# Performance work log

Measured on AMD Instinct MI355X. Metric: run time of the kernel, lower is better.

## Reference

```python
import jax, jax.numpy as jnp
import numpy as np
from jax.ops import segment_sum

N = 100000
E = 1600000
IN_C = 128
WIDTHS = [128, 64, 32, 16, 8]  # hidden_feats=128 -> /1,/2,/4,/8,/16


def setup_inputs() -> dict:
    key = jax.random.key(0)
    ks = jax.random.split(key, 12)
    x = jax.random.normal(ks[0], (N, IN_C), dtype=jnp.float32)
    edge_index = jax.random.randint(ks[1], (2, E), 0, N, dtype=jnp.int64)
    inp = {"x": x, "edge_index": edge_index}
    fan_in = [IN_C] + WIDTHS[:-1]
    for i, (fi, fo) in enumerate(zip(fan_in, WIDTHS)):
        # Glorot init like PyG GCNConv
        lim = float(np.sqrt(6.0 / (fi + fo)))
        inp[f"W{i+1}"] = jax.random.uniform(ks[2 + i], (fi, fo), dtype=jnp.float32, minval=-lim, maxval=lim)
        inp[f"b{i+1}"] = jnp.zeros((fo,), dtype=jnp.float32)
    return inp


def _gcn_norm(edge_index):
    # add self loops, compute D^{-1/2} (A+I) D^{-1/2} edge weights
    loops = jnp.arange(N, dtype=edge_index.dtype)
    src = jnp.concatenate([edge_index[0], loops])  # [E+N]
    dst = jnp.concatenate([edge_index[1], loops])
    deg = segment_sum(jnp.ones_like(dst, dtype=jnp.float32), dst, num_segments=N)
    dinv = jnp.where(deg > 0, jax.lax.rsqrt(jnp.maximum(deg, 1.0)), 0.0)
    norm = dinv[src] * dinv[dst]  # [E+N]
    return src, dst, norm


def _gcn_layer(x, W, b, src, dst, norm):
    h = x @ W                         # [N, Fout] linear transform first (PyG order)
    msg = h[src] * norm[:, None]      # gather + edge scaling, [E+N, Fout]
    out = segment_sum(msg, dst, num_segments=N)  # scatter-add aggregation
    return out + b


def reference(x, edge_index, W1, b1, W2, b2, W3, b3, W4, b4, W5, b5):
    src, dst, norm = _gcn_norm(edge_index)
    params = [(W1, b1), (W2, b2), (W3, b3), (W4, b4), (W5, b5)]
    h = x
    for W, b in params:
        h = jax.nn.relu(_gcn_layer(h, W, b, src, dst, norm))
    return h
```

## Files before the change

kernel.cpp:

```cpp
#include <hip/hip_runtime.h>
#include <hip/hip_bf16.h>
#include <hip/hip_fp16.h>


#define LDSE8  4096
#define LDSE16 2048
#define PCHUNK 4096
#define BNODES 512
#define MAXBUK 256

typedef float floatx4 __attribute__((ext_vector_type(4)));
typedef _Float16 f16x4 __attribute__((ext_vector_type(4)));
typedef _Float16 f16x8 __attribute__((ext_vector_type(8)));

__global__ __launch_bounds__(256) void k_bucket(const int* __restrict__ src,
                                                const int* __restrict__ dst,
                                                int2* __restrict__ pairs,
                                                int* __restrict__ bcnt,
                                                int E, int nbk, int CAP) {
    __shared__ int  hist[MAXBUK], pre[MAXBUK], cur[MAXBUK], gbase[MAXBUK], tmp[MAXBUK];
    __shared__ int2 arena[PCHUNK];
    const int tid = threadIdx.x;
    const int e0  = blockIdx.x * PCHUNK;
    const int m   = (E - e0 < PCHUNK) ? (E - e0) : PCHUNK;

    hist[tid] = 0;
    __syncthreads();

    int dl[PCHUNK / 256], sl[PCHUNK / 256], rl[PCHUNK / 256];
#pragma unroll
    for (int j = 0; j < PCHUNK / 256; ++j) {
        int i = j * 256 + tid;
        rl[j] = -1;
        if (i < m) {
            dl[j] = __builtin_nontemporal_load(&dst[e0 + i]);
            sl[j] = __builtin_nontemporal_load(&src[e0 + i]);
            rl[j] = dl[j] >> 9;
            atomicAdd(&hist[rl[j]], 1);
        }
    }
    __syncthreads();
    int v = hist[tid];
    tmp[tid] = v;
    __syncthreads();
    for (int off = 1; off < MAXBUK; off <<= 1) {
        int t = (tid >= off) ? tmp[tid - off] : 0;
        __syncthreads();
        tmp[tid] += t;
        __syncthreads();
    }
    pre[tid] = tmp[tid] - v;
    cur[tid] = 0;
    __syncthreads();
#pragma unroll
    for (int j = 0; j < PCHUNK / 256; ++j) {
        if (rl[j] >= 0) {
            int slot = pre[rl[j]] + atomicAdd(&cur[rl[j]], 1);
            arena[slot] = make_int2(dl[j], sl[j]);
        }
    }
    __syncthreads();
    if (tid < nbk && hist[tid] > 0) gbase[tid] = atomicAdd(&bcnt[tid], hist[tid]);
    __syncthreads();
    const int wave = tid >> 6, lane = tid & 63;
    for (int r = wave; r < nbk; r += 4) {
        int cnt = hist[r];
        if (cnt == 0) continue;
        int b0 = pre[r], g = gbase[r];
        for (int j = lane; j < cnt; j += 64)
            pairs[(size_t)r * CAP + g + j] = arena[b0 + j];
    }
}

__global__ void k_bscan(const int* __restrict__ bcnt, int* __restrict__ bbase,
                        int* __restrict__ offsets, int nbk, int n, int E) {
    __shared__ int tmp[MAXBUK];
    const int tid = threadIdx.x;
    int v = (tid < nbk) ? bcnt[tid] : 0;
    tmp[tid] = v;
    __syncthreads();
    for (int off = 1; off < MAXBUK; off <<= 1) {
        int t = (tid >= off) ? tmp[tid - off] : 0;
        __syncthreads();
        tmp[tid] += t;
        __syncthreads();
    }
    if (tid < nbk) bbase[tid] = tmp[tid] - v;
    if (tid == 0) offsets[n] = E;
}

__global__ __launch_bounds__(256) void k_sortfill(const int2* __restrict__ pairs,
                                                  const int* __restrict__ bcnt,
                                                  const int* __restrict__ bbase,
                                                  int* __restrict__ csr_src,
                                                  int* __restrict__ offsets,
                                                  float* __restrict__ dinv,
                                                  int n, int CAP) {
    __shared__ int hist[BNODES], lofs[BNODES], cur[BNODES], tmp[256];
    const int r    = blockIdx.x;
    const int tid  = threadIdx.x;
    const int m    = bcnt[r];
    const int base = bbase[r];
    const int node0 = r * BNODES;
    const int2* p = pairs + (size_t)r * CAP;

    for (int l = tid; l < BNODES; l += 256) hist[l] = 0;
    __syncthreads();
    for (int i = tid; i < m; i += 256)
        atomicAdd(&hist[p[i].x - node0], 1);
    __syncthreads();
    int a = hist[2 * tid], b = hist[2 * tid + 1];
    int s = a + b;
    tmp[tid] = s;
    __syncthreads();
    for (int off = 1; off < 256; off <<= 1) {
        int t = (tid >= off) ? tmp[tid - off] : 0;
        __syncthreads();
        tmp[tid] += t;
        __syncthreads();
    }
    int exc = tmp[tid] - s;
    lofs[2 * tid]     = exc;
    lofs[2 * tid + 1] = exc + a;
    cur[2 * tid] = 0;
    cur[2 * tid + 1] = 0;
    __syncthreads();
    for (int i = tid; i < m; i += 256) {
        int2 e = p[i];
        int l = e.x - node0;
        int pos = lofs[l] + atomicAdd(&cur[l], 1);
        csr_src[base + pos] = e.y;
    }
    for (int l = tid; l < BNODES; l += 256) {
        int node = node0 + l;
        if (node < n) {
            offsets[node] = base + lofs[l];
            dinv[node]    = rsqrtf((float)(hist[l] + 1));
        }
    }
}

template <int FIN, int FOUT, bool BIN>
__global__ __launch_bounds__(512) void k_mgemm(const float* __restrict__ x,
                                               const float* __restrict__ W,
                                               const float* __restrict__ dinv,
                                               _Float16* __restrict__ g, int n) {
    constexpr int KC  = (FIN < 64) ? FIN : 64;
    constexpr int NKQ = KC / 4;
    constexpr int AP  = KC + 4;
    constexpr int NT  = FOUT / 16;
    __shared__ _Float16 As[128 * AP];
    __shared__ _Float16 Ws[FOUT * AP];
    __shared__ float dv[128];

    const int tid  = threadIdx.x;
    const int wave = tid >> 6;
    const int lane = tid & 63;
    const int m0   = blockIdx.x * 128;
    const floatx4* x4 = reinterpret_cast<const floatx4*>(x);

    if (tid < 128) dv[tid] = (m0 + tid < n) ? dinv[m0 + tid] : 0.f;

    floatx4 acc[NT];
#pragma unroll
    for (int t = 0; t < NT; ++t) acc[t] = (floatx4)(0.f);

    for (int kc0 = 0; kc0 < FIN; kc0 += KC) {
        __syncthreads();
        for (int s = tid; s < 128 * NKQ; s += 512) {
            int node = s / NKQ, kq = s % NKQ;
            int gn = m0 + node, gslot = kc0 / 4 + kq;
            floatx4 v = (floatx4)(0.f);
            if (gn < n) {
                size_t idx = BIN ? (((size_t)(gslot >> 2) * n + gn) * 4 + (gslot & 3))
                                 : ((size_t)gn * (FIN / 4) + gslot);
                v = __builtin_nontemporal_load(&x4[idx]);
            }
            f16x4 h = {(_Float16)v.x, (_Float16)v.y, (_Float16)v.z, (_Float16)v.w};
            *reinterpret_cast<f16x4*>(&As[node * AP + kq * 4]) = h;
        }
        for (int s = tid; s < FOUT * NKQ; s += 512) {
            int fo = s % FOUT, kq = s / FOUT;
            int k = kc0 + kq * 4;
            f16x4 h = {(_Float16)W[(k + 0) * FOUT + fo], (_Float16)W[(k + 1) * FOUT + fo],
                       (_Float16)W[(k + 2) * FOUT + fo], (_Float16)W[(k + 3) * FOUT + fo]};
            *reinterpret_cast<f16x4*>(&Ws[fo * AP + kq * 4]) = h;
        }
        __syncthreads();
#pragma unroll
        for (int kk = 0; kk < KC / 32; ++kk) {
            const int ka = kk * 32 + ((lane >> 4) << 2);
            const _Float16* ap = &As[(wave * 16 + (lane & 15)) * AP + ka];
            f16x4 alo = *reinterpret_cast<const f16x4*>(ap);
            f16x4 ahi = *reinterpret_cast<const f16x4*>(ap + 16);
            f16x8 a = {alo[0], alo[1], alo[2], alo[3], ahi[0], ahi[1], ahi[2], ahi[3]};
#pragma unroll
            for (int t = 0; t < NT; ++t) {
                const _Float16* bp = &Ws[(t * 16 + (lane & 15)) * AP + ka];
                f16x4 blo = *reinterpret_cast<const f16x4*>(bp);
                f16x4 bhi = *reinterpret_cast<const f16x4*>(bp + 16);
                f16x8 b = {blo[0], blo[1], blo[2], blo[3], bhi[0], bhi[1], bhi[2], bhi[3]};
                acc[t] = __builtin_amdgcn_mfma_f32_16x16x32_f16(a, b, acc[t], 0, 0, 0);
            }
        }
    }

    const int i0 = (lane >> 4) << 2;
#pragma unroll
    for (int r = 0; r < 4; ++r) {
        int nl = wave * 16 + i0 + r;
        int node = m0 + nl;
        if (node < n) {
            float d = dv[nl];
#pragma unroll
            for (int t = 0; t < NT; ++t) {
                int fo = t * 16 + (lane & 15);
                g[((size_t)(fo >> 5) * n + node) * 32 + (fo & 31)] = (_Float16)(acc[t][r] * d);
            }
        }
    }
}

template <int FIN, int FOUT, int NR, int NC>
__global__ __launch_bounds__(256) void k_gemm(const float* __restrict__ x,
                                              const float* __restrict__ W,
                                              const float* __restrict__ dinv,
                                              float* __restrict__ g, int n) {
    constexpr int NFG = FOUT / NC;
    constexpr int M   = NR * (256 / NFG);
    constexpr int KC  = (FIN < 32) ? FIN : 32;
    constexpr int MP  = M + 4;
    constexpr int WP  = KC * NC + 4;
    __shared__ float Wl[NFG * WP];
    __shared__ float xt[KC * MP];

    const int tid = threadIdx.x;
    const int fg  = tid % NFG;
    const int mg  = tid / NFG;
    const int m0  = blockIdx.x * M;
    const floatx4* x4 = reinterpret_cast<const floatx4*>(x);

    float acc[NR][NC];
#pragma unroll
    for (int i = 0; i < NR; ++i)
#pragma unroll
        for (int j = 0; j < NC; ++j) acc[i][j] = 0.f;

    for (int kc0 = 0; kc0 < FIN; kc0 += KC) {
        __syncthreads();
        for (int idx = tid; idx < KC * FOUT; idx += 256) {
            int k  = idx / FOUT;
            int fo = idx % FOUT;
            Wl[(fo / NC) * WP + k * NC + (fo % NC)] = W[(kc0 + k) * FOUT + fo];
        }
        constexpr int SLOTS = KC / 4;
        for (int s = tid; s < M * SLOTS; s += 256) {
            int ml    = s / SLOTS;
            int slot  = s % SLOTS;
            int gslot = kc0 / 4 + slot;
            int gn    = m0 + ml;
            floatx4 v = (floatx4)(0.f);
            if (gn < n) {
                size_t idx2 = ((size_t)(gslot >> 2) * n + gn) * 4 + (gslot & 3);
                v = __builtin_nontemporal_load(&x4[idx2]);
            }
            xt[(slot * 4 + 0) * MP + ml] = v.x;
            xt[(slot * 4 + 1) * MP + ml] = v.y;
            xt[(slot * 4 + 2) * MP + ml] = v.z;
            xt[(slot * 4 + 3) * MP + ml] = v.w;
        }
        __syncthreads();
#pragma unroll 4
        for (int k = 0; k < KC; ++k) {
            float xr[NR], wr[NC];
#pragma unroll
            for (int p = 0; p < NR / 4; ++p) {
                float4 v = *reinterpret_cast<const float4*>(&xt[k * MP + mg * NR + p * 4]);
                xr[p * 4 + 0] = v.x; xr[p * 4 + 1] = v.y;
                xr[p * 4 + 2] = v.z; xr[p * 4 + 3] = v.w;
            }
#pragma unroll
            for (int p = 0; p < NC / 4; ++p) {
                float4 v = *reinterpret_cast<const float4*>(&Wl[fg * WP + k * NC + p * 4]);
                wr[p * 4 + 0] = v.x; wr[p * 4 + 1] = v.y;
                wr[p * 4 + 2] = v.z; wr[p * 4 + 3] = v.w;
            }
#pragma unroll
            for (int i = 0; i < NR; ++i)
#pragma unroll
                for (int j = 0; j < NC; ++j) acc[i][j] += xr[i] * wr[j];
        }
    }

    float4* g4 = reinterpret_cast<float4*>(g);
#pragma unroll
    for (int i = 0; i < NR; ++i) {
        int gn = m0 + mg * NR + i;
        if (gn < n) {
            float d = dinv[gn];
#pragma unroll
            for (int p = 0; p < NC / 4; ++p) {
                float4 o = make_float4(acc[i][p * 4 + 0] * d, acc[i][p * 4 + 1] * d,
                                       acc[i][p * 4 + 2] * d, acc[i][p * 4 + 3] * d);
                int slot = (fg * NC) / 4 + p;
                if constexpr (FOUT >= 16)
                    g4[((size_t)(slot >> 2) * n + gn) * 4 + (slot & 3)] = o;
                else
                    g4[(size_t)gn * 2 + slot] = o;
            }
        }
    }
}

#define ACCUM8(A, v) {                                                        \
    union { float4 f; __half2 h[4]; } u_; u_.f = (v);                         \
    _Pragma("unroll")                                                         \
    for (int j_ = 0; j_ < 4; ++j_) {                                          \
        float2 f_ = __half22float2(u_.h[j_]);                                 \
        A[2 * j_] += f_.x; A[2 * j_ + 1] += f_.y;                             \
    } }

__global__ __launch_bounds__(256) void k_aggrh(const float4* __restrict__ gh,
                                               const int* __restrict__ offsets,
                                               const int* __restrict__ csr_src,
                                               const float* __restrict__ dinv,
                                               const float* __restrict__ bias,
                                               float4* __restrict__ outb,
                                               int n, int nsl) {
    __shared__ int eidx[LDSE16];
    const int sl     = blockIdx.x % nsl;
    const int nb     = blockIdx.x / nsl;
    const int node0  = nb * 64;
    const int nodeHi = (node0 + 64 < n) ? node0 + 64 : n;
    const int node   = node0 + (threadIdx.x >> 2);
    const int q      = threadIdx.x & 3;

    const int eS = offsets[node0];
    const int eE = offsets[nodeHi];
    const int C  = eE - eS;
    const bool useLds = (C <= LDSE16);

    const bool alive = (node < n);
    int e0 = 0, e1 = 0;
    float dnode = 0.f;
    const float4* gs = gh + (size_t)sl * n * 4;
    float A[8], B[8];
#pragma unroll
    for (int j = 0; j < 8; ++j) { A[j] = 0.f; B[j] = 0.f; }
    if (alive) {
        e0 = offsets[node];
        e1 = offsets[node + 1];
        dnode = dinv[node];
        float4 vs = gs[(size_t)node * 4 + q];
        ACCUM8(A, vs);
    }

    if (useLds) {
        for (int i = threadIdx.x; i < C; i += 256)
            eidx[i] = __builtin_nontemporal_load(&csr_src[eS + i]);
    }
    __syncthreads();
    if (!alive) return;

    const int m = e1 - e0;
    int i = 0;
    if (useLds) {
        const int le = e0 - eS;
        for (; i + 4 <= m; i += 4) {
            int s0 = eidx[le + i + 0], s1 = eidx[le + i + 1];
            int s2 = eidx[le + i + 2], s3 = eidx[le + i + 3];
            float4 v0 = gs[(size_t)s0 * 4 + q], v1 = gs[(size_t)s1 * 4 + q];
            float4 v2 = gs[(size_t)s2 * 4 + q], v3 = gs[(size_t)s3 * 4 + q];
            ACCUM8(A, v0); ACCUM8(B, v1); ACCUM8(A, v2); ACCUM8(B, v3);
        }
        for (; i < m; ++i) {
            float4 v = gs[(size_t)eidx[le + i] * 4 + q];
            ACCUM8(A, v);
        }
    } else {
        for (; i + 4 <= m; i += 4) {
            int s0 = csr_src[e0 + i + 0], s1 = csr_src[e0 + i + 1];
            int s2 = csr_src[e0 + i + 2], s3 = csr_src[e0 + i + 3];
            float4 v0 = gs[(size_t)s0 * 4 + q], v1 = gs[(size_t)s1 * 4 + q];
            float4 v2 = gs[(size_t)s2 * 4 + q], v3 = gs[(size_t)s3 * 4 + q];
            ACCUM8(A, v0); ACCUM8(B, v1); ACCUM8(A, v2); ACCUM8(B, v3);
        }
        for (; i < m; ++i) {
            float4 v = gs[(size_t)csr_src[e0 + i] * 4 + q];
            ACCUM8(A, v);
        }
    }

    const float* bf = bias + sl * 32 + q * 8;
    floatx4 r0, r1;
    r0.x = fmaxf(dnode * (A[0] + B[0]) + bf[0], 0.f);
    r0.y = fmaxf(dnode * (A[1] + B[1]) + bf[1], 0.f);
    r0.z = fmaxf(dnode * (A[2] + B[2]) + bf[2], 0.f);
    r0.w = fmaxf(dnode * (A[3] + B[3]) + bf[3], 0.f);
    r1.x = fmaxf(dnode * (A[4] + B[4]) + bf[4], 0.f);
    r1.y = fmaxf(dnode * (A[5] + B[5]) + bf[5], 0.f);
    r1.z = fmaxf(dnode * (A[6] + B[6]) + bf[6], 0.f);
    r1.w = fmaxf(dnode * (A[7] + B[7]) + bf[7], 0.f);
    floatx4* ob = reinterpret_cast<floatx4*>(outb);
    size_t base = ((size_t)(sl * 2 + (q >> 1)) * n + node) * 4 + (q & 1) * 2;
    __builtin_nontemporal_store(r0, &ob[base + 0]);
    __builtin_nontemporal_store(r1, &ob[base + 1]);
}

__global__ __launch_bounds__(256) void k_aggr16(const float4* __restrict__ gb,
                                                const int* __restrict__ offsets,
                                                const int* __restrict__ csr_src,
                                                const float* __restrict__ dinv,
                                                const float* __restrict__ bias,
                                                float4* __restrict__ outb,
                                                int n, int nsl) {
    __shared__ int eidx[LDSE16];
    const int sl     = blockIdx.x % nsl;
    const int nb     = blockIdx.x / nsl;
    const int node0  = nb * 64;
    const int nodeHi = (node0 + 64 < n) ? node0 + 64 : n;
    const int node   = node0 + (threadIdx.x >> 2);
    const int q      = threadIdx.x & 3;

    const int eS = offsets[node0];
    const int eE = offsets[nodeHi];
    const int C  = eE - eS;
    const bool useLds = (C <= LDSE16);

    const bool alive = (node < n);
    int e0 = 0, e1 = 0;
    float dnode = 0.f;
    const float4* gs = gb + (size_t)sl * n * 4;
    float4 a0 = make_float4(0.f, 0.f, 0.f, 0.f);
    if (alive) {
        e0 = offsets[node];
        e1 = offsets[node + 1];
        dnode = dinv[node];
        a0 = gs[(size_t)node * 4 + q];
    }

    if (useLds) {
        for (int i = threadIdx.x; i < C; i += 256)
            eidx[i] = __builtin_nontemporal_load(&csr_src[eS + i]);
    }
    __syncthreads();
    if (!alive) return;

    float4 a1 = make_float4(0.f, 0.f, 0.f, 0.f);
    float4 a2 = a1, a3 = a1;

    const int m = e1 - e0;
    int i = 0;
    if (useLds) {
        const int le = e0 - eS;
        for (; i + 4 <= m; i += 4) {
            int s0 = eidx[le + i + 0], s1 = eidx[le + i + 1];
            int s2 = eidx[le + i + 2], s3 = eidx[le + i + 3];
            float4 v0 = gs[(size_t)s0 * 4 + q], v1 = gs[(size_t)s1 * 4 + q];
            float4 v2 = gs[(size_t)s2 * 4 + q], v3 = gs[(size_t)s3 * 4 + q];
            a0.x += v0.x; a0.y += v0.y; a0.z += v0.z; a0.w += v0.w;
            a1.x += v1.x; a1.y += v1.y; a1.z += v1.z; a1.w += v1.w;
            a2.x += v2.x; a2.y += v2.y; a2.z += v2.z; a2.w += v2.w;
            a3.x += v3.x; a3.y += v3.y; a3.z += v3.z; a3.w += v3.w;
        }
        for (; i < m; ++i) {
            float4 v = gs[(size_t)eidx[le + i] * 4 + q];
            a0.x += v.x; a0.y += v.y; a0.z += v.z; a0.w += v.w;
        }
    } else {
        for (; i < m; ++i) {
            float4 v = gs[(size_t)csr_src[e0 + i] * 4 + q];
            a0.x += v.x; a0.y += v.y; a0.z += v.z; a0.w += v.w;
        }
    }
    a0.x += a1.x + a2.x + a3.x;
    a0.y += a1.y + a2.y + a3.y;
    a0.z += a1.z + a2.z + a3.z;
    a0.w += a1.w + a2.w + a3.w;

    const float* bf = bias + sl * 16 + q * 4;
    floatx4 r;
    r.x = fmaxf(dnode * a0.x + bf[0], 0.f);
    r.y = fmaxf(dnode * a0.y + bf[1], 0.f);
    r.z = fmaxf(dnode * a0.z + bf[2], 0.f);
    r.w = fmaxf(dnode * a0.w + bf[3], 0.f);
    floatx4* ob = reinterpret_cast<floatx4*>(outb);
    __builtin_nontemporal_store(r, &ob[((size_t)sl * n + node) * 4 + q]);
}

__global__ __launch_bounds__(256) void k_aggr8(const float4* __restrict__ gb,
                                               const int* __restrict__ offsets,
                                               const int* __restrict__ csr_src,
                                               const float* __restrict__ dinv,
                                               const float* __restrict__ bias,
                                               float4* __restrict__ outb, int n) {
    __shared__ int eidx[LDSE8];
    const int node0  = blockIdx.x * 128;
    const int nodeHi = (node0 + 128 < n) ? node0 + 128 : n;
    const int node   = node0 + (threadIdx.x >> 1);
    const int h      = threadIdx.x & 1;

    const int eS = offsets[node0];
    const int eE = offsets[nodeHi];
    const int C  = eE - eS;
    const bool useLds = (C <= LDSE8);

    const bool alive = (node < n);
    int e0 = 0, e1 = 0;
    float dnode = 0.f;
    float4 a0 = make_float4(0.f, 0.f, 0.f, 0.f);
    if (alive) {
        e0 = offsets[node];
        e1 = offsets[node + 1];
        dnode = dinv[node];
        a0 = gb[(size_t)node * 2 + h];
    }

    if (useLds) {
        for (int i = threadIdx.x; i < C; i += 256)
            eidx[i] = __builtin_nontemporal_load(&csr_src[eS + i]);
    }
    __syncthreads();
    if (!alive) return;

    float4 a1 = make_float4(0.f, 0.f, 0.f, 0.f);
    float4 a2 = a1, a3 = a1;

    const int m = e1 - e0;
    int i = 0;
    if (useLds) {
        const int le = e0 - eS;
        for (; i + 4 <= m; i += 4) {
            int s0 = eidx[le + i + 0], s1 = eidx[le + i + 1];
            int s2 = eidx[le + i + 2], s3 = eidx[le + i + 3];
            float4 v0 = gb[(size_t)s0 * 2 + h], v1 = gb[(size_t)s1 * 2 + h];
            float4 v2 = gb[(size_t)s2 * 2 + h], v3 = gb[(size_t)s3 * 2 + h];
            a0.x += v0.x; a0.y += v0.y; a0.z += v0.z; a0.w += v0.w;
            a1.x += v1.x; a1.y += v1.y; a1.z += v1.z; a1.w += v1.w;
            a2.x += v2.x; a2.y += v2.y; a2.z += v2.z; a2.w += v2.w;
            a3.x += v3.x; a3.y += v3.y; a3.z += v3.z; a3.w += v3.w;
        }
        for (; i < m; ++i) {
            float4 v = gb[(size_t)eidx[le + i] * 2 + h];
            a0.x += v.x; a0.y += v.y; a0.z += v.z; a0.w += v.w;
        }
    } else {
        for (; i < m; ++i) {
            float4 v = gb[(size_t)csr_src[e0 + i] * 2 + h];
            a0.x += v.x; a0.y += v.y; a0.z += v.z; a0.w += v.w;
        }
    }
    a0.x += a1.x + a2.x + a3.x;
    a0.y += a1.y + a2.y + a3.y;
    a0.z += a1.z + a2.z + a3.z;
    a0.w += a1.w + a2.w + a3.w;

    const float* bf = bias + h * 4;
    floatx4 r;
    r.x = fmaxf(dnode * a0.x + bf[0], 0.f);
    r.y = fmaxf(dnode * a0.y + bf[1], 0.f);
    r.z = fmaxf(dnode * a0.z + bf[2], 0.f);
    r.w = fmaxf(dnode * a0.w + bf[3], 0.f);
    floatx4* ob = reinterpret_cast<floatx4*>(outb);
    __builtin_nontemporal_store(r, &ob[(size_t)node * 2 + h]);
}

extern "C" void kernel_launch(void* const* d_in, const int* in_sizes, int n_in,
                              void* d_out, int out_size, void* d_ws, size_t ws_size,
                              hipStream_t stream) {
    const int N = in_sizes[0] / 128;
    const int E = in_sizes[1] / 2;
    const int nbk = (N + BNODES - 1) / BNODES;
    const int avg = (E + nbk - 1) / nbk;
    const int CAP = avg + avg / 4 + 512;

    const float* x   = (const float*)d_in[0];
    const int*   ei  = (const int*)d_in[1];
    const int*   src = ei;
    const int*   dst = ei + E;
    const float* W1 = (const float*)d_in[2],  *b1 = (const float*)d_in[3];
    const float* W2 = (const float*)d_in[4],  *b2 = (const float*)d_in[5];
    const float* W3 = (const float*)d_in[6],  *b3 = (const float*)d_in[7];
    const float* W4 = (const float*)d_in[8],  *b4 = (const float*)d_in[9];
    const float* W5 = (const float*)d_in[10], *b5 = (const float*)d_in[11];
    float* out = (float*)d_out;

    size_t off = 0;
    auto alloc = [&](size_t bytes) {
        void* p = (char*)d_ws + off;
        off += (bytes + 255) & ~(size_t)255;
        return p;
    };
    int*   offsets = (int*)alloc((size_t)(N + 1) * 4);
    float* dinv    = (float*)alloc((size_t)N * 4);
    int*   csr_src = (int*)alloc((size_t)E * 4);
    int*   bcnt    = (int*)alloc(MAXBUK * 4);
    int*   bbase   = (int*)alloc(MAXBUK * 4);
    int2*  pairs   = (int2*)alloc((size_t)nbk * CAP * 8);
    float* g       = (float*)alloc((size_t)N * 128 * 4);
    float* xbuf    = (float*)alloc((size_t)N * 128 * 4);

    (void)hipMemsetAsync(bcnt, 0, MAXBUK * 4, stream);

    const int TB = 256;
    int nb16 = (N + 63) / 64;
    int nb8  = (N + 127) / 128;
    int nbm  = (N + 127) / 128;
    int nch  = (E + PCHUNK - 1) / PCHUNK;

    k_bucket<<<nch, TB, 0, stream>>>(src, dst, pairs, bcnt, E, nbk, CAP);
    k_bscan<<<1, MAXBUK, 0, stream>>>(bcnt, bbase, offsets, nbk, N, E);
    k_sortfill<<<nbk, TB, 0, stream>>>(pairs, bcnt, bbase, csr_src, offsets, dinv, N, CAP);

    const float4* g4  = (const float4*)g;
    float4*       xb4 = (float4*)xbuf;
    _Float16*     gh  = (_Float16*)g;

    k_mgemm<128, 128, false><<<nbm, 512, 0, stream>>>(x, W1, dinv, gh, N);
    k_aggrh<<<nb16 * 4, TB, 0, stream>>>(g4, offsets, csr_src, dinv, b1, xb4, N, 4);
    k_mgemm<128, 64, true><<<nbm, 512, 0, stream>>>(xbuf, W2, dinv, gh, N);
    k_aggrh<<<nb16 * 2, TB, 0, stream>>>(g4, offsets, csr_src, dinv, b2, xb4, N, 2);
    k_mgemm<64, 32, true><<<nbm, 512, 0, stream>>>(xbuf, W3, dinv, gh, N);
    k_aggrh<<<nb16 * 1, TB, 0, stream>>>(g4, offsets, csr_src, dinv, b3, xb4, N, 1);
    k_gemm<32, 16, 4, 4><<<(N + 255) / 256, TB, 0, stream>>>(xbuf, W4, dinv, (float*)g, N);
    k_aggr16<<<nb16 * 1, TB, 0, stream>>>(g4, offsets, csr_src, dinv, b4, xb4, N, 1);
    k_gemm<16, 8, 4, 4><<<(N + 511) / 512, TB, 0, stream>>>(xbuf, W5, dinv, (float*)g, N);
    k_aggr8<<<nb8, TB, 0, stream>>>(g4, offsets, csr_src, dinv, b5, (float4*)out, N);
}
```

Measured before the change: 380.1 us.

## Store layer-1/2 aggregation outputs as fp16 and read them directly in GEMM

The aggregation kernel for layers 1 and 2 now writes its ReLU output as fp16 in a sliced layout of 32 features. The next GEMM loads that fp16 data directly with 8-wide vector loads instead of reading fp32 and converting it. This halves the intermediate activation traffic between those kernels. The change also unrolls the LDS-index gather loop to 8 edges per iteration and widens the LDS row padding, which adds some rounding of intermediate activations to fp16 and extra register pressure.

After: 380.3 us. Within noise of the previous version (+0.1%).

```diff
diff --git a/kernel.cpp b/kernel.cpp
--- a/kernel.cpp
+++ b/kernel.cpp
@@ -140,14 +140,14 @@
     }
 }
 
-template <int FIN, int FOUT, bool BIN>
+template <int FIN, int FOUT, bool H16IN>
 __global__ __launch_bounds__(512) void k_mgemm(const float* __restrict__ x,
                                                const float* __restrict__ W,
                                                const float* __restrict__ dinv,
                                                _Float16* __restrict__ g, int n) {
     constexpr int KC  = (FIN < 64) ? FIN : 64;
     constexpr int NKQ = KC / 4;
-    constexpr int AP  = KC + 4;
+    constexpr int AP  = KC + 8;
     constexpr int NT  = FOUT / 16;
     __shared__ _Float16 As[128 * AP];
     __shared__ _Float16 Ws[FOUT * AP];
@@ -157,7 +157,6 @@
     const int wave = tid >> 6;
     const int lane = tid & 63;
     const int m0   = blockIdx.x * 128;
-    const floatx4* x4 = reinterpret_cast<const floatx4*>(x);
 
     if (tid < 128) dv[tid] = (m0 + tid < n) ? dinv[m0 + tid] : 0.f;
 
@@ -167,17 +166,29 @@
 
     for (int kc0 = 0; kc0 < FIN; kc0 += KC) {
         __syncthreads();
-        for (int s = tid; s < 128 * NKQ; s += 512) {
-            int node = s / NKQ, kq = s % NKQ;
-            int gn = m0 + node, gslot = kc0 / 4 + kq;
-            floatx4 v = (floatx4)(0.f);
-            if (gn < n) {
-                size_t idx = BIN ? (((size_t)(gslot >> 2) * n + gn) * 4 + (gslot & 3))
-                                 : ((size_t)gn * (FIN / 4) + gslot);
-                v = __builtin_nontemporal_load(&x4[idx]);
-            }
-            f16x4 h = {(_Float16)v.x, (_Float16)v.y, (_Float16)v.z, (_Float16)v.w};
-            *reinterpret_cast<f16x4*>(&As[node * AP + kq * 4]) = h;
+        if constexpr (H16IN) {
+            const _Float16* xh = reinterpret_cast<const _Float16*>(x);
+            constexpr int NC8 = KC / 8;
+            for (int s = tid; s < 128 * NC8; s += 512) {
+                int node = s / NC8, c8 = s % NC8;
+                int gn = m0 + node, f0 = kc0 + c8 * 8;
+                f16x8 h = (f16x8)(_Float16)0;
+                if (gn < n)
+                    h = *reinterpret_cast<const f16x8*>(
+                        &xh[((size_t)(f0 >> 5) * n + gn) * 32 + (f0 & 31)]);
+                *reinterpret_cast<f16x8*>(&As[node * AP + c8 * 8]) = h;
+            }
+        } else {
+            const floatx4* x4 = reinterpret_cast<const floatx4*>(x);
+            for (int s = tid; s < 128 * NKQ; s += 512) {
+                int node = s / NKQ, kq = s % NKQ;
+                int gn = m0 + node, gslot = kc0 / 4 + kq;
+                floatx4 v = (floatx4)(0.f);
+                if (gn < n)
+                    v = __builtin_nontemporal_load(&x4[(size_t)gn * (FIN / 4) + gslot]);
+                f16x4 h = {(_Float16)v.x, (_Float16)v.y, (_Float16)v.z, (_Float16)v.w};
+                *reinterpret_cast<f16x4*>(&As[node * AP + kq * 4]) = h;
+            }
         }
         for (int s = tid; s < FOUT * NKQ; s += 512) {
             int fo = s % FOUT, kq = s / FOUT;
@@ -320,6 +331,7 @@
         A[2 * j_] += f_.x; A[2 * j_ + 1] += f_.y;                             \
     } }
 
+template <bool H16OUT>
 __global__ __launch_bounds__(256) void k_aggrh(const float4* __restrict__ gh,
                                                const int* __restrict__ offsets,
                                                const int* __restrict__ csr_src,
@@ -366,6 +378,18 @@
     int i = 0;
     if (useLds) {
         const int le = e0 - eS;
+        for (; i + 8 <= m; i += 8) {
+            int s0 = eidx[le + i + 0], s1 = eidx[le + i + 1];
+            int s2 = eidx[le + i + 2], s3 = eidx[le + i + 3];
+            int s4 = eidx[le + i + 4], s5 = eidx[le + i + 5];
+            int s6 = eidx[le + i + 6], s7 = eidx[le + i + 7];
+            float4 v0 = gs[(size_t)s0 * 4 + q], v1 = gs[(size_t)s1 * 4 + q];
+            float4 v2 = gs[(size_t)s2 * 4 + q], v3 = gs[(size_t)s3 * 4 + q];
+            float4 v4 = gs[(size_t)s4 * 4 + q], v5 = gs[(size_t)s5 * 4 + q];
+            float4 v6 = gs[(size_t)s6 * 4 + q], v7 = gs[(size_t)s7 * 4 + q];
+            ACCUM8(A, v0); ACCUM8(B, v1); ACCUM8(A, v2); ACCUM8(B, v3);
+            ACCUM8(A, v4); ACCUM8(B, v5); ACCUM8(A, v6); ACCUM8(B, v7);
+        }
         for (; i + 4 <= m; i += 4) {
             int s0 = eidx[le + i + 0], s1 = eidx[le + i + 1];
             int s2 = eidx[le + i + 2], s3 = eidx[le + i + 3];
@@ -392,19 +416,26 @@
     }
 
     const float* bf = bias + sl * 32 + q * 8;
-    floatx4 r0, r1;
-    r0.x = fmaxf(dnode * (A[0] + B[0]) + bf[0], 0.f);
-    r0.y = fmaxf(dnode * (A[1] + B[1]) + bf[1], 0.f);
-    r0.z = fmaxf(dnode * (A[2] + B[2]) + bf[2], 0.f);
-    r0.w = fmaxf(dnode * (A[3] + B[3]) + bf[3], 0.f);
-    r1.x = fmaxf(dnode * (A[4] + B[4]) + bf[4], 0.f);
-    r1.y = fmaxf(dnode * (A[5] + B[5]) + bf[5], 0.f);
-    r1.z = fmaxf(dnode * (A[6] + B[6]) + bf[6], 0.f);
-    r1.w = fmaxf(dnode * (A[7] + B[7]) + bf[7], 0.f);
-    floatx4* ob = reinterpret_cast<floatx4*>(outb);
-    size_t base = ((size_t)(sl * 2 + (q >> 1)) * n + node) * 4 + (q & 1) * 2;
-    __builtin_nontemporal_store(r0, &ob[base + 0]);
-    __builtin_nontemporal_store(r1, &ob[base + 1]);
+    float r[8];
+#pragma unroll
+    for (int j = 0; j < 8; ++j)
+        r[j] = fmaxf(dnode * (A[j] + B[j]) + bf[j], 0.f);
+
+    if constexpr (H16OUT) {
+        f16x8 o;
+#pragma unroll
+        for (int j = 0; j < 8; ++j) o[j] = (_Float16)r[j];
+        _Float16* oh = reinterpret_cast<_Float16*>(outb);
+        __builtin_nontemporal_store(
+            o, reinterpret_cast<f16x8*>(&oh[((size_t)sl * n + node) * 32 + q * 8]));
+    } else {
+        floatx4 r0 = {r[0], r[1], r[2], r[3]};
+        floatx4 r1 = {r[4], r[5], r[6], r[7]};
+        floatx4* ob = reinterpret_cast<floatx4*>(outb);
+        size_t base = ((size_t)(sl * 2 + (q >> 1)) * n + node) * 4 + (q & 1) * 2;
+        __builtin_nontemporal_store(r0, &ob[base + 0]);
+        __builtin_nontemporal_store(r1, &ob[base + 1]);
+    }
 }
 
 __global__ __launch_bounds__(256) void k_aggr16(const float4* __restrict__ gb,
@@ -617,11 +648,11 @@
     _Float16*     gh  = (_Float16*)g;
 
     k_mgemm<128, 128, false><<<nbm, 512, 0, stream>>>(x, W1, dinv, gh, N);
-    k_aggrh<<<nb16 * 4, TB, 0, stream>>>(g4, offsets, csr_src, dinv, b1, xb4, N, 4);
+    k_aggrh<true><<<nb16 * 4, TB, 0, stream>>>(g4, offsets, csr_src, dinv, b1, xb4, N, 4);
     k_mgemm<128, 64, true><<<nbm, 512, 0, stream>>>(xbuf, W2, dinv, gh, N);
-    k_aggrh<<<nb16 * 2, TB, 0, stream>>>(g4, offsets, csr_src, dinv, b2, xb4, N, 2);
+    k_aggrh<true><<<nb16 * 2, TB, 0, stream>>>(g4, offsets, csr_src, dinv, b2, xb4, N, 2);
     k_mgemm<64, 32, true><<<nbm, 512, 0, stream>>>(xbuf, W3, dinv, gh, N);
-    k_aggrh<<<nb16 * 1, TB, 0, stream>>>(g4, offsets, csr_src, dinv, b3, xb4, N, 1);
+    k_aggrh<false><<<nb16 * 1, TB, 0, stream>>>(g4, offsets, csr_src, dinv, b3, xb4, N, 1);
     k_gemm<32, 16, 4, 4><<<(N + 255) / 256, TB, 0, stream>>>(xbuf, W4, dinv, (float*)g, N);
     k_aggr16<<<nb16 * 1, TB, 0, stream>>>(g4, offsets, csr_src, dinv, b4, xb4, N, 1);
     k_gemm<16, 8, 4, 4><<<(N + 511) / 512, TB, 0, stream>>>(xbuf, W5, dinv, (float*)g, N);
```
